# Performance work log

Measured on AMD Instinct MI355X. Metric: run time of the kernel, lower is better.

## Reference

```python
import jax, jax.numpy as jnp
import numpy as np


def _conv3x3(x, w):
    # x: [N,C,H,W], w: [O,I,3,3], stride 1, padding 1 -> SAME
    return jax.lax.conv_general_dilated(
        x, w, window_strides=(1, 1), padding='SAME',
        dimension_numbers=('NCHW', 'OIHW', 'NCHW'))


def setup_inputs() -> dict:
    key = jax.random.key(0)
    k1, k2, k3, k4 = jax.random.split(key, 4)
    # He-like init scale for 3x3 convs
    x = jax.random.normal(k1, (8, 1, 512, 512), dtype=jnp.float32)
    w1 = jax.random.normal(k2, (8, 1, 3, 3), dtype=jnp.float32) * (2.0 / (1 * 9)) ** 0.5
    wmid = jax.random.normal(k3, (18, 8, 8, 3, 3), dtype=jnp.float32) * (2.0 / (8 * 9)) ** 0.5
    w20 = jax.random.normal(k4, (1, 8, 3, 3), dtype=jnp.float32) * (2.0 / (8 * 9)) ** 0.5
    return {'x': x, 'w1': w1, 'wmid': wmid, 'w20': w20}


def reference(x, w1, wmid, w20):
    y = jax.nn.relu(_conv3x3(x, w1))  # conv1 + relu
    # conv2..conv19: 18 identical 8->8 conv+relu layers, scanned over stacked weights
    def body(y, w):
        return jax.nn.relu(_conv3x3(y, w)), None
    y, _ = jax.lax.scan(body, y, wmid)
    return _conv3x3(y, w20)  # conv20, no relu
```

## Files before the change

kernel.cpp:

```cpp
#include <hip/hip_runtime.h>

typedef _Float16 f16;
typedef _Float16 f16x8 __attribute__((ext_vector_type(8)));
typedef _Float16 f16x4 __attribute__((ext_vector_type(4)));
typedef float v4f __attribute__((ext_vector_type(4)));

constexpr int H = 512, W = 512, NB = 8;
constexpr int ROWS = 514;
constexpr int COLS = 528;
constexpr int CH = 8;
constexpr size_t ROWBYTES = (size_t)COLS * CH * 2;
constexpr size_t PLANE_ELEMS = (size_t)ROWS * COLS * CH;
constexpr size_t PLANE_BYTES = PLANE_ELEMS * 2;

constexpr int RSP = 145;
constexpr int RSPC = RSP * CH;
constexpr int LDS_ROWB = RSP * 16;
constexpr int WTAB_L = 3072;

constexpr int FRSP = 81;
constexpr int FRSPC = FRSP * CH;
constexpr int FROWB = FRSP * 16;
constexpr int INR = 12;
constexpr int ARR = 10;

__device__ __forceinline__ void gload_lds16(const void* g, void* l) {
    __builtin_amdgcn_global_load_lds(
        (const __attribute__((address_space(1))) unsigned int*)g,
        (__attribute__((address_space(3))) unsigned int*)l, 16, 0, 0);
}
__device__ __forceinline__ void gload_lds4(const void* g, void* l) {
    __builtin_amdgcn_global_load_lds(
        (const __attribute__((address_space(1))) unsigned int*)g,
        (__attribute__((address_space(3))) unsigned int*)l, 4, 0, 0);
}

__global__ void zero_borders(f16* __restrict__ base, size_t set_stride) {
    const int i = blockIdx.x * 256 + threadIdx.x;
    if (i >= 9248) return;
    const int img = blockIdx.y, set = blockIdx.z;
    int row, col;
    if (i < 1056) { row = (i < 528) ? 0 : 513; col = (i < 528) ? i : i - 528; }
    else {
        const int j = i - 1056;
        row = 1 + (j >> 4);
        const int c4 = j & 15;
        col = (c4 < 8) ? c4 : 512 + c4;
    }
    f16x8 z = {};
    f16* p = base + (size_t)set * set_stride + ((size_t)img * ROWS + row) * COLS * CH + (size_t)col * CH;
    *(f16x8*)p = z;
}

__global__ void build_wtab(const float* __restrict__ wmid,
                           const float* __restrict__ w20,
                           f16* __restrict__ wtab) {
    const int l = blockIdx.x;
    const int lane = threadIdx.x;
    const float* wt = (l < 18) ? wmid + (size_t)l * 576 : w20;
    const int COUT = (l < 18) ? 8 : 1;
    const int n = lane & 15, q = lane >> 4;
#pragma unroll
    for (int g = 0; g < 3; ++g) {
        const int t = g * 4 + q;
        f16x8 hv, lv;
#pragma unroll
        for (int j = 0; j < 8; ++j) {
            float wv = 0.f;
            if (n < 8) {
                if (t <= 8 && n < COUT) wv = wt[(n * 8 + j) * 9 + t];
            } else {
                const int o = n - 8;
                if (t >= 3 && o < COUT) wv = wt[(o * 8 + j) * 9 + (t - 3)];
            }
            const f16 h = (f16)wv;
            hv[j] = h;
            lv[j] = (f16)(wv - (float)h);
        }
        f16* dst = wtab + (size_t)l * WTAB_L + (g * 2) * 512 + lane * 8;
        *(f16x8*)dst = hv;
        *(f16x8*)(dst + 512) = lv;
    }
}

__global__ __launch_bounds__(256) void conv1_kernel(
    const float* __restrict__ in, const float* __restrict__ wt,
    f16* __restrict__ out)
{
    const int x0 = (blockIdx.x * 64 + threadIdx.x) * 4;
    const int y  = blockIdx.y * 4 + threadIdx.y;
    const int b  = blockIdx.z;
    const float* inb = in + (size_t)b * H * W;

    float patch[3][6];
#pragma unroll
    for (int r = 0; r < 3; ++r) {
        const int iy = y - 1 + r;
        if (iy >= 0 && iy < H) {
            const float* rp = inb + (size_t)iy * W;
            const float4 v = *(const float4*)(rp + x0);
            patch[r][1] = v.x; patch[r][2] = v.y; patch[r][3] = v.z; patch[r][4] = v.w;
            patch[r][0] = (x0 > 0)     ? rp[x0 - 1] : 0.f;
            patch[r][5] = (x0 + 4 < W) ? rp[x0 + 4] : 0.f;
        } else {
#pragma unroll
            for (int k = 0; k < 6; ++k) patch[r][k] = 0.f;
        }
    }

    float acc[8][4];
#pragma unroll
    for (int o = 0; o < 8; ++o) {
        const float* wo = wt + o * 9;
        float a0 = 0.f, a1 = 0.f, a2 = 0.f, a3 = 0.f;
#pragma unroll
        for (int r = 0; r < 3; ++r)
#pragma unroll
            for (int k = 0; k < 3; ++k) {
                const float wv = wo[r * 3 + k];
                a0 = fmaf(wv, patch[r][k + 0], a0);
                a1 = fmaf(wv, patch[r][k + 1], a1);
                a2 = fmaf(wv, patch[r][k + 2], a2);
                a3 = fmaf(wv, patch[r][k + 3], a3);
            }
        acc[o][0] = a0; acc[o][1] = a1; acc[o][2] = a2; acc[o][3] = a3;
    }

#pragma unroll
    for (int j = 0; j < 4; ++j) {
        f16x8 hv;
#pragma unroll
        for (int o = 0; o < 8; ++o)
            hv[o] = (f16)fmaxf(acc[o][j], 0.f);
        const size_t off = (((size_t)b * ROWS + (y + 1)) * COLS + (x0 + j + 8)) * CH;
        *(f16x8*)(out + off) = hv;
    }
}

__global__ __launch_bounds__(256, 4) void conv2fused(
    const f16* __restrict__ in,
    const f16* __restrict__ wtA, const f16* __restrict__ wtB,
    f16* __restrict__ outp)
{
    __shared__ __align__(16) f16 aring[ARR * FRSPC];
    __shared__ __align__(16) f16 inring[INR * FRSPC];

    const int wave = threadIdx.x >> 6, lane = threadIdx.x & 63;
    const int img = blockIdx.x, xt = blockIdx.y;
    const int x0 = xt * 64;
    const int base = blockIdx.z * 32;

    f16x8 ahiW[3], aloW[3], bhiW[3], bloW[3];
#pragma unroll
    for (int g = 0; g < 3; ++g) {
        const f16* wa = wtA + (g * 2) * 512 + lane * 8;
        ahiW[g] = *(const f16x8*)wa;  aloW[g] = *(const f16x8*)(wa + 512);
        const f16* wb = wtB + (g * 2) * 512 + lane * 8;
        bhiW[g] = *(const f16x8*)wb;  bloW[g] = *(const f16x8*)(wb + 512);
    }

    const char* src = (const char*)in + (size_t)img * PLANE_BYTES + (size_t)x0 * 16;

    auto stage = [&](int r0, int cnt) {
        for (int rr = wave; rr < cnt; rr += 4) {
            const int row = r0 + rr;
            const int rowc = min(max(row, 0), 513);
            const int slot = ((row % INR) + INR) % INR;
            const char* gs = src + (size_t)rowc * ROWBYTES;
            char* ld = (char*)inring + slot * FROWB;
            gload_lds16(gs + lane * 16, ld);
            if (lane < 16) gload_lds16(gs + 1024 + lane * 16, ld + 1024);
        }
    };

    const int n = lane & 15, q = lane >> 4;
    int tyv[3], txv[3];
#pragma unroll
    for (int g = 0; g < 3; ++g) { const int t = g * 4 + q; tyv[g] = t / 3 - 1; txv[g] = t % 3 - 1; }
    const int rowoff = q >> 1, choff = (q & 1) * 4;
    const bool xe0 = (xt == 0), xe7 = (xt == 7);

    auto computeA = [&](int rA) {
        int irow[3];
#pragma unroll
        for (int g = 0; g < 3; ++g) {
            const int r = rA + tyv[g];
            irow[g] = (((r % INR) + INR) % INR) * FRSPC;
        }
        const int gyA = rA + rowoff;
        const int wrow = (gyA % ARR) * FRSPC;
        const bool zr = (gyA == 0) || (gyA == 513);
#pragma unroll
        for (int s = 0; s < 5; ++s) {
            v4f acc = {0.f,0.f,0.f,0.f}, acc2 = {0.f,0.f,0.f,0.f};
#pragma unroll
            for (int g = 0; g < 3; ++g) {
                const f16x8 xv = *(const f16x8*)&inring[irow[g] + (16 * s + n + txv[g]) * CH];
                acc  = __builtin_amdgcn_mfma_f32_16x16x32_f16(ahiW[g], xv, acc,  0, 0, 0);
                acc2 = __builtin_amdgcn_mfma_f32_16x16x32_f16(aloW[g], xv, acc2, 0, 0, 0);
            }
            const v4f res = acc + acc2;
            f16x4 hv;
#pragma unroll
            for (int c = 0; c < 4; ++c) hv[c] = (f16)fmaxf(res[c], 0.f);
            if (zr || (xe0 && s == 0 && n == 7) || (xe7 && s == 4 && n == 8)) {
                hv[0] = (f16)0.f; hv[1] = (f16)0.f; hv[2] = (f16)0.f; hv[3] = (f16)0.f;
            }
            *(f16x4*)&aring[wrow + (16 * s + n) * CH + choff] = hv;
        }
    };

    auto computeB = [&](int rB) {
        int brow[3];
#pragma unroll
        for (int g = 0; g < 3; ++g) brow[g] = ((rB + tyv[g]) % ARR) * FRSPC;
        const int gyB = rB + rowoff;
        f16* orow = outp + ((size_t)img * ROWS + gyB) * COLS * CH + (size_t)(x0 + 8) * CH + choff;
#pragma unroll
        for (int s = 0; s < 4; ++s) {
            v4f acc = {0.f,0.f,0.f,0.f}, acc2 = {0.f,0.f,0.f,0.f};
#pragma unroll
            for (int g = 0; g < 3; ++g) {
                const f16x8 xv = *(const f16x8*)&aring[brow[g] + (16 * s + n + txv[g] + 8) * CH];
                acc  = __builtin_amdgcn_mfma_f32_16x16x32_f16(bhiW[g], xv, acc,  0, 0, 0);
                acc2 = __builtin_amdgcn_mfma_f32_16x16x32_f16(bloW[g], xv, acc2, 0, 0, 0);
            }
            const v4f res = acc + acc2;
            f16x4 hv;
#pragma unroll
            for (int c = 0; c < 4; ++c) hv[c] = (f16)fmaxf(res[c], 0.f);
            *(f16x4*)(orow + (size_t)(16 * s + n) * CH) = hv;
        }
    };

    stage(base - 1, 12);
    __syncthreads();
    if (wave == 0) computeA(base);

    for (int t = 0; t < 4; ++t) {
        computeA(base + 8 * t + 2 + 2 * wave);
        __syncthreads();
        if (t < 3) stage(base + 8 * t + 11, 8);
        computeB(base + 8 * t + 1 + 2 * wave);
        __syncthreads();
    }
}

template<bool RELU, bool FINAL>
__global__ __launch_bounds__(256) void convmfma(
    const f16* __restrict__ in, const f16* __restrict__ wtab_l,
    f16* __restrict__ outp, float* __restrict__ out_final)
{
    __shared__ __align__(16) f16 lds[2][10 * RSPC];

    const int wave = threadIdx.x >> 6, lane = threadIdx.x & 63;
    const int img = blockIdx.x;
    const int x0 = blockIdx.y * 128;
    const int ybase = blockIdx.z * 32;

    f16x8 bhi[3], blo[3];
#pragma unroll
    for (int g = 0; g < 3; ++g) {
        const f16* wp = wtab_l + (g * 2) * 512 + lane * 8;
        bhi[g] = *(const f16x8*)wp;
        blo[g] = *(const f16x8*)(wp + 512);
    }

    const char* src = (const char*)in + (size_t)img * PLANE_BYTES + (size_t)x0 * 16;
    auto stage = [&](int buf, int y0) {
        char* dst = (char*)&lds[buf][0];
        for (int qq = wave; qq < 30; qq += 4) {
            const int r = qq / 3, c = qq % 3;
            const char* gs = src + (size_t)(y0 + r) * ROWBYTES;
            char* ld = dst + r * LDS_ROWB;
            if (c < 2) gload_lds16(gs + c * 1024 + lane * 16, ld + c * 1024);
            else       gload_lds4(gs + 2048 + lane * 4, ld + 2048);
        }
    };

    const int n = lane & 15, q = lane >> 4, m = lane & 15;
    int abase[3];
#pragma unroll
    for (int g = 0; g < 3; ++g) {
        const int t = g * 4 + q;
        const int ty = t / 3 - 1, tx = t % 3 - 1;
        abase[g] = (2 * wave + ty + 1) * RSP + (m + tx + 8);
    }
    const int rowoff = q >> 1;
    const int choff = (q & 1) * 4;

    stage(0, ybase);
    __syncthreads();

    for (int t = 0; t < 4; ++t) {
        if (t < 3) stage((t + 1) & 1, ybase + 8 * (t + 1));
        const f16* L = &lds[t & 1][0];
        const int Y = ybase + 8 * t + 2 * wave;
#pragma unroll
        for (int s = 0; s < 8; ++s) {
            v4f acc = {0.f,0.f,0.f,0.f}, acc2 = {0.f,0.f,0.f,0.f};
#pragma unroll
            for (int g = 0; g < 3; ++g) {
                const f16x8 xv = *(const f16x8*)&L[(abase[g] + 16 * s) * CH];
                acc  = __builtin_amdgcn_mfma_f32_16x16x32_f16(bhi[g], xv, acc,  0, 0, 0);
                acc2 = __builtin_amdgcn_mfma_f32_16x16x32_f16(blo[g], xv, acc2, 0, 0, 0);
            }
            const v4f res = acc + acc2;
            if constexpr (!FINAL) {
                f16x4 hv;
#pragma unroll
                for (int c = 0; c < 4; ++c) {
                    float v = res[c];
                    if (RELU) v = fmaxf(v, 0.f);
                    hv[c] = (f16)v;
                }
                const int gy = Y + rowoff + 1;
                const int gx = x0 + 16 * s + n + 8;
                *(f16x4*)(outp + ((size_t)img * ROWS + gy) * COLS * CH + (size_t)gx * CH + choff) = hv;
            } else {
                if ((q & 1) == 0) {
                    const int gy = Y + rowoff, gx = x0 + 16 * s + n;
                    out_final[((size_t)img * H + gy) * W + gx] = res[0];
                }
            }
        }
        if (t < 3) __syncthreads();
    }
}

extern "C" void kernel_launch(void* const* d_in, const int* in_sizes, int n_in,
                              void* d_out, int out_size, void* d_ws, size_t ws_size,
                              hipStream_t stream) {
    const float* x    = (const float*)d_in[0];
    const float* w1   = (const float*)d_in[1];
    const float* wmid = (const float*)d_in[2];
    const float* w20  = (const float*)d_in[3];
    float* out = (float*)d_out;

    const size_t wtab_bytes = (size_t)19 * WTAB_L * 2;
    int g = NB;
    while (g > 1 && 2 * (size_t)g * PLANE_BYTES + wtab_bytes > ws_size) g >>= 1;

    f16* act0 = (f16*)d_ws;
    f16* act1 = act0 + (size_t)g * PLANE_ELEMS;
    f16* wtab = act1 + (size_t)g * PLANE_ELEMS;

    zero_borders<<<dim3(37, g, 2), 256, 0, stream>>>(act0, (size_t)g * PLANE_ELEMS);
    build_wtab<<<19, 64, 0, stream>>>(wmid, w20, wtab);

    for (int b0 = 0; b0 < NB; b0 += g) {
        conv1_kernel<<<dim3(2, 128, g), dim3(64, 4), 0, stream>>>(
            x + (size_t)b0 * H * W, w1, act0);
        for (int k = 0; k < 9; ++k) {
            const f16* s0 = (k & 1) ? act1 : act0;
            f16*       d0 = (k & 1) ? act0 : act1;
            conv2fused<<<dim3(g, 8, 16), 256, 0, stream>>>(
                s0, wtab + (size_t)(2 * k) * WTAB_L, wtab + (size_t)(2 * k + 1) * WTAB_L, d0);
        }
        convmfma<false, true><<<dim3(g, 4, 16), 256, 0, stream>>>(
            act1, wtab + (size_t)18 * WTAB_L, nullptr, out + (size_t)b0 * H * W);
    }
}
```

Measured before the change: 274.3 us.

## Fuse three middle conv layers per kernel instead of two

Replaces the two-layer fused conv kernel with a three-layer version that keeps two intermediate activations in LDS ring buffers, cutting the 9 mid-layer launches to 6. This reduces global-memory round trips of the fp16 activation planes between layers. In exchange each tile recomputes more halo rows and columns, LDS usage grows with the extra ring, the prologue schedule becomes more complex, and register pressure rises from holding a third weight set.

After: 332.1 us. 1.21x slower.

```diff
diff --git a/kernel.cpp b/kernel.cpp
--- a/kernel.cpp
+++ b/kernel.cpp
@@ -23,6 +23,9 @@
 constexpr int FROWB = FRSP * 16;
 constexpr int INR = 12;
 constexpr int ARR = 10;
+constexpr int BRR = 10;
+constexpr int BRSP = 69;
+constexpr int BRSPC = BRSP * CH;
 
 __device__ __forceinline__ void gload_lds16(const void* g, void* l) {
     __builtin_amdgcn_global_load_lds(
@@ -137,11 +140,12 @@
     }
 }
 
-__global__ __launch_bounds__(256, 4) void conv2fused(
+__global__ __launch_bounds__(256, 4) void conv3fused(
     const f16* __restrict__ in,
     const f16* __restrict__ wtA, const f16* __restrict__ wtB,
-    f16* __restrict__ outp)
+    const f16* __restrict__ wtC, f16* __restrict__ outp)
 {
+    __shared__ __align__(16) f16 bring[BRR * BRSPC];
     __shared__ __align__(16) f16 aring[ARR * FRSPC];
     __shared__ __align__(16) f16 inring[INR * FRSPC];
 
@@ -150,27 +154,29 @@
     const int x0 = xt * 64;
     const int base = blockIdx.z * 32;
 
-    f16x8 ahiW[3], aloW[3], bhiW[3], bloW[3];
+    f16x8 ahiW[3], aloW[3], bhiW[3], bloW[3], chiW[3], cloW[3];
 #pragma unroll
     for (int g = 0; g < 3; ++g) {
         const f16* wa = wtA + (g * 2) * 512 + lane * 8;
         ahiW[g] = *(const f16x8*)wa;  aloW[g] = *(const f16x8*)(wa + 512);
         const f16* wb = wtB + (g * 2) * 512 + lane * 8;
         bhiW[g] = *(const f16x8*)wb;  bloW[g] = *(const f16x8*)(wb + 512);
+        const f16* wc = wtC + (g * 2) * 512 + lane * 8;
+        chiW[g] = *(const f16x8*)wc;  cloW[g] = *(const f16x8*)(wc + 512);
     }
 
     const char* src = (const char*)in + (size_t)img * PLANE_BYTES + (size_t)x0 * 16;
 
+    auto stage_row = [&](int row) {
+        const int rowc = min(max(row, 0), 513);
+        const int slot = ((row % INR) + INR) % INR;
+        const char* gs = src + (size_t)rowc * ROWBYTES;
+        char* ld = (char*)inring + slot * FROWB;
+        gload_lds16(gs + lane * 16, ld);
+        if (lane < 16) gload_lds16(gs + 1024 + lane * 16, ld + 1024);
+    };
     auto stage = [&](int r0, int cnt) {
-        for (int rr = wave; rr < cnt; rr += 4) {
-            const int row = r0 + rr;
-            const int rowc = min(max(row, 0), 513);
-            const int slot = ((row % INR) + INR) % INR;
-            const char* gs = src + (size_t)rowc * ROWBYTES;
-            char* ld = (char*)inring + slot * FROWB;
-            gload_lds16(gs + lane * 16, ld);
-            if (lane < 16) gload_lds16(gs + 1024 + lane * 16, ld + 1024);
-        }
+        for (int rr = wave; rr < cnt; rr += 4) stage_row(r0 + rr);
     };
 
     const int n = lane & 15, q = lane >> 4;
@@ -188,7 +194,7 @@
             irow[g] = (((r % INR) + INR) % INR) * FRSPC;
         }
         const int gyA = rA + rowoff;
-        const int wrow = (gyA % ARR) * FRSPC;
+        const int wrow = (((gyA % ARR) + ARR) % ARR) * FRSPC;
         const bool zr = (gyA == 0) || (gyA == 513);
 #pragma unroll
         for (int s = 0; s < 5; ++s) {
@@ -211,19 +217,54 @@
     };
 
     auto computeB = [&](int rB) {
+        int arow[3];
+#pragma unroll
+        for (int g = 0; g < 3; ++g) {
+            const int r = rB + tyv[g];
+            arow[g] = (((r % ARR) + ARR) % ARR) * FRSPC;
+        }
+        const int gyB = rB + rowoff;
+        const int wrow = (((gyB % BRR) + BRR) % BRR) * BRSPC;
+        const bool zr = (gyB == 0) || (gyB == 513);
+#pragma unroll
+        for (int s = 0; s < 5; ++s) {
+            v4f acc = {0.f,0.f,0.f,0.f}, acc2 = {0.f,0.f,0.f,0.f};
+#pragma unroll
+            for (int g = 0; g < 3; ++g) {
+                const f16x8 xv = *(const f16x8*)&aring[arow[g] + (16 * s + n + txv[g]) * CH];
+                acc  = __builtin_amdgcn_mfma_f32_16x16x32_f16(bhiW[g], xv, acc,  0, 0, 0);
+                acc2 = __builtin_amdgcn_mfma_f32_16x16x32_f16(bloW[g], xv, acc2, 0, 0, 0);
+            }
+            const v4f res = acc + acc2;
+            f16x4 hv;
+#pragma unroll
+            for (int c = 0; c < 4; ++c) hv[c] = (f16)fmaxf(res[c], 0.f);
+            if (zr || (xe0 && s == 0 && n == 7) || (xe7 && s == 4 && n == 8)) {
+                hv[0] = (f16)0.f; hv[1] = (f16)0.f; hv[2] = (f16)0.f; hv[3] = (f16)0.f;
+            }
+            const int c16 = 16 * s + n;
+            if (c16 >= 6 && c16 <= 73)
+                *(f16x4*)&bring[wrow + (c16 - 6) * CH + choff] = hv;
+        }
+    };
+
+    auto computeC = [&](int rC) {
         int brow[3];
 #pragma unroll
-        for (int g = 0; g < 3; ++g) brow[g] = ((rB + tyv[g]) % ARR) * FRSPC;
-        const int gyB = rB + rowoff;
-        f16* orow = outp + ((size_t)img * ROWS + gyB) * COLS * CH + (size_t)(x0 + 8) * CH + choff;
+        for (int g = 0; g < 3; ++g) {
+            const int r = rC + tyv[g];
+            brow[g] = (((r % BRR) + BRR) % BRR) * BRSPC;
+        }
+        const int gyC = rC + rowoff;
+        f16* orow = outp + ((size_t)img * ROWS + gyC) * COLS * CH + (size_t)(x0 + 8) * CH + choff;
 #pragma unroll
         for (int s = 0; s < 4; ++s) {
             v4f acc = {0.f,0.f,0.f,0.f}, acc2 = {0.f,0.f,0.f,0.f};
 #pragma unroll
             for (int g = 0; g < 3; ++g) {
-                const f16x8 xv = *(const f16x8*)&aring[brow[g] + (16 * s + n + txv[g] + 8) * CH];
-                acc  = __builtin_amdgcn_mfma_f32_16x16x32_f16(bhiW[g], xv, acc,  0, 0, 0);
-                acc2 = __builtin_amdgcn_mfma_f32_16x16x32_f16(bloW[g], xv, acc2, 0, 0, 0);
+                const f16x8 xv = *(const f16x8*)&bring[brow[g] + (16 * s + n + txv[g] + 2) * CH];
+                acc  = __builtin_amdgcn_mfma_f32_16x16x32_f16(chiW[g], xv, acc,  0, 0, 0);
+                acc2 = __builtin_amdgcn_mfma_f32_16x16x32_f16(cloW[g], xv, acc2, 0, 0, 0);
             }
             const v4f res = acc + acc2;
             f16x4 hv;
@@ -233,15 +274,26 @@
         }
     };
 
-    stage(base - 1, 12);
-    __syncthreads();
-    if (wave == 0) computeA(base);
+    stage(base - 2, 12);
+    __syncthreads();
+    for (int p = wave; p < 5; p += 4) computeA(base - 1 + 2 * p);
+    __syncthreads();
+    stage(base + 10, 8);
+    computeB(base + 2 * wave);
+    __syncthreads();
+    if (wave == 0)      computeA(base + 9);
+    else if (wave >= 2) stage_row(base + 16 + wave);
+    __syncthreads();
+    if (wave == 0) computeB(base + 8);
+    __syncthreads();
 
     for (int t = 0; t < 4; ++t) {
-        computeA(base + 8 * t + 2 + 2 * wave);
+        if (t < 3) computeA(base + 11 + 8 * t + 2 * wave);
+        computeC(base + 1 + 8 * t + 2 * wave);
+        if (t == 3) break;
         __syncthreads();
-        if (t < 3) stage(base + 8 * t + 11, 8);
-        computeB(base + 8 * t + 1 + 2 * wave);
+        if (t < 2) stage(base + 20 + 8 * t, 8);
+        computeB(base + 10 + 8 * t + 2 * wave);
         __syncthreads();
     }
 }
@@ -351,13 +403,17 @@
     for (int b0 = 0; b0 < NB; b0 += g) {
         conv1_kernel<<<dim3(2, 128, g), dim3(64, 4), 0, stream>>>(
             x + (size_t)b0 * H * W, w1, act0);
-        for (int k = 0; k < 9; ++k) {
+        for (int k = 0; k < 6; ++k) {
             const f16* s0 = (k & 1) ? act1 : act0;
             f16*       d0 = (k & 1) ? act0 : act1;
-            conv2fused<<<dim3(g, 8, 16), 256, 0, stream>>>(
-                s0, wtab + (size_t)(2 * k) * WTAB_L, wtab + (size_t)(2 * k + 1) * WTAB_L, d0);
+            conv3fused<<<dim3(g, 8, 16), 256, 0, stream>>>(
+                s0,
+                wtab + (size_t)(3 * k)     * WTAB_L,
+                wtab + (size_t)(3 * k + 1) * WTAB_L,
+                wtab + (size_t)(3 * k + 2) * WTAB_L,
+                d0);
         }
         convmfma<false, true><<<dim3(g, 4, 16), 256, 0, stream>>>(
-            act1, wtab + (size_t)18 * WTAB_L, nullptr, out + (size_t)b0 * H * W);
-    }
-}
+            act0, wtab + (size_t)18 * WTAB_L, nullptr, out + (size_t)b0 * H * W);
+    }
+}
```
